# Kernel optimization log

Measured on AMD Instinct MI355X. Metric: run time of the kernel, lower is better.

Reference implementation:

```python
import jax, jax.numpy as jnp
import numpy as np

B, C, NS, NT = 8, 256, 16384, 2048
KQ = 64            # self-attention key/query dim
D = 64             # cond_conv_feat_dim
W0, W1, W2 = D * D, D * D, D * 1   # dynamic weight sizes (predict_mask=True)
B0, B1, B2 = D, D, 1
CTRL = W0 + W1 + W2 + B0 + B1 + B2  # 8385


def setup_inputs() -> dict:
    key = jax.random.key(0)
    ks = jax.random.split(key, 9)
    return {
        "scene_feat": jax.random.normal(ks[0], (B, C, NS), jnp.float32),
        "template_feat": jax.random.normal(ks[1], (B, C, NT), jnp.float32),
        # SelfAttention 1x1-conv (= linear over channels) weights
        "q_w": jax.random.normal(ks[2], (KQ, C), jnp.float32) * 0.02,
        "k_w": jax.random.normal(ks[3], (KQ, C), jnp.float32) * 0.02,
        "v_w": jax.random.normal(ks[4], (C, C), jnp.float32) * 0.02,
        # projection head of SimpleAggregator: Conv1d(3*C -> D, k=1) + ReLU
        "proj_w": jax.random.normal(ks[5], (D, 3 * C), jnp.float32) * 0.02,
        "proj_b": jnp.zeros((D,), jnp.float32),
        # controller head: Linear(C -> CTRL), init normal(std=0.01), bias 0
        "ctrl_w": jax.random.normal(ks[6], (CTRL, C), jnp.float32) * 0.01,
        "ctrl_b": jnp.zeros((CTRL,), jnp.float32),
    }


def _self_attention(x, q_w, k_w, v_w):
    # x: [B, C, N] -> [B, C_out, N]
    q = jnp.einsum("kc,bcn->bnk", q_w, x)          # [B, N, KQ]
    k = jnp.einsum("kc,bcn->bkn", k_w, x)          # [B, KQ, N]
    v = jnp.einsum("oc,bcn->bno", v_w, x)          # [B, N, C_out]
    attn = jax.nn.softmax(jnp.einsum("bnk,bkm->bnm", q / jnp.sqrt(jnp.float32(KQ)), k), axis=-1)
    y = jnp.einsum("bnm,bmo->bon", attn, v)        # [B, C_out, N]
    return y


def reference(scene_feat, template_feat, q_w, k_w, v_w, proj_w, proj_b, ctrl_w, ctrl_b):
    # ---- SimpleAggregator (self-attention on template inside) ----
    t_sa = _self_attention(template_feat, q_w, k_w, v_w)       # [B, C, NT]
    t_max = jnp.max(t_sa, axis=-1, keepdims=True)              # [B, C, 1]
    aggr = jnp.concatenate(
        [scene_feat - t_max, scene_feat * t_max, scene_feat], axis=1
    )                                                          # [B, 3C, NS]
    x = jax.nn.relu(jnp.einsum("oc,bcn->bon", proj_w, aggr) + proj_b[None, :, None])  # [B, D, NS]

    # ---- controller head on ORIGINAL template_feat max-pooled ----
    pooled = jnp.max(template_feat, axis=-1)                   # [B, C]
    params = pooled @ ctrl_w.T + ctrl_b                        # [B, CTRL]

    # parse_dynamic_params: splits = weights then biases
    o = 0
    w0 = params[:, o:o + W0].reshape(B, D, D); o += W0
    w1 = params[:, o:o + W1].reshape(B, D, D); o += W1
    w2 = params[:, o:o + W2].reshape(B, 1, D); o += W2
    b0 = params[:, o:o + B0]; o += B0
    b1 = params[:, o:o + B1]; o += B1
    b2 = params[:, o:o + B2]

    # per-sample dynamic 1x1 convs (groups=batch trick == batched GEMM)
    x = jax.nn.relu(jnp.einsum("boi,bin->bon", w0, x) + b0[:, :, None])
    x = jax.nn.relu(jnp.einsum("boi,bin->bon", w1, x) + b1[:, :, None])
    x = jnp.einsum("boi,bin->bon", w2, x) + b2[:, :, None]    # [B, 1, NS], no relu (mask layer)
    return x.reshape(B, NS)
```

## Files before the change

kernel.cpp:

```cpp
#include <hip/hip_runtime.h>
#include <hip/hip_fp8.h>


typedef __attribute__((ext_vector_type(8))) short short8;
typedef __attribute__((ext_vector_type(4))) short short4v;
typedef __attribute__((ext_vector_type(4))) float f32x4;

__device__ __forceinline__ unsigned short f2bf(float f){
  unsigned u = __float_as_uint(f);
  u += 0x7FFFu + ((u >> 16) & 1u);
  return (unsigned short)(u >> 16);
}
__device__ __forceinline__ unsigned char f2e4m3(float f){
  return __hip_fp8_e4m3(f).__x;
}
__device__ __forceinline__ unsigned fenc(float f){
  unsigned u = __float_as_uint(f);
  return (u & 0x80000000u) ? ~u : (u | 0x80000000u);
}
__device__ __forceinline__ float fdec(unsigned k){
  unsigned u = (k & 0x80000000u) ? (k & 0x7FFFFFFFu) : ~k;
  return __uint_as_float(u);
}

__global__ __launch_bounds__(256) void k0w(const float* __restrict__ qw,
    const float* __restrict__ kw, const float* __restrict__ vw,
    unsigned short* __restrict__ Wbf, unsigned* __restrict__ tmaxe,
    unsigned* __restrict__ pooledEnc){
  if (blockIdx.x == 0){
    const unsigned ninf = fenc(-3.0e38f);
    for (int i = threadIdx.x; i < 2048; i += 256){
      tmaxe[i] = 0u;
      pooledEnc[i] = ninf;
    }
  }
  const int e = (blockIdx.x * 256 + threadIdx.x) * 4;
  const int row = e >> 8, c = e & 255;
  const float* src;
  float scl = 1.0f;
  if (row < 64){ src = qw + row * 256 + c; scl = 0.125f; }
  else if (row < 128){ src = kw + (row - 64) * 256 + c; }
  else { src = vw + (row - 128) * 256 + c; }
  float4 v = *(const float4*)src;
  short4v o;
  o[0] = (short)f2bf(v.x * scl); o[1] = (short)f2bf(v.y * scl);
  o[2] = (short)f2bf(v.z * scl); o[3] = (short)f2bf(v.w * scl);
  *(short4v*)(Wbf + e) = o;
}

__global__ __launch_bounds__(256) void k0_tt(const float* __restrict__ T,
    unsigned short* __restrict__ Tt, unsigned* __restrict__ pooledEnc){
  const int b = blockIdx.x, nt = blockIdx.y, ct = blockIdx.z;
  const int n0 = nt * 128, c0 = ct * 32;
  const int tid = threadIdx.x;
  __shared__ float Ls[32][129];
  const int cr = tid >> 3, nq = tid & 7;
  const float* src = T + ((size_t)b * 256 + c0 + cr) * 2048 + n0 + nq * 16;
  float4 v0 = ((const float4*)src)[0];
  float4 v1 = ((const float4*)src)[1];
  float4 v2 = ((const float4*)src)[2];
  float4 v3 = ((const float4*)src)[3];
  float mx = fmaxf(fmaxf(fmaxf(v0.x, v0.y), fmaxf(v0.z, v0.w)),
                   fmaxf(fmaxf(v1.x, v1.y), fmaxf(v1.z, v1.w)));
  mx = fmaxf(mx, fmaxf(fmaxf(fmaxf(v2.x, v2.y), fmaxf(v2.z, v2.w)),
                       fmaxf(fmaxf(v3.x, v3.y), fmaxf(v3.z, v3.w))));
  mx = fmaxf(mx, __shfl_xor(mx, 1));
  mx = fmaxf(mx, __shfl_xor(mx, 2));
  mx = fmaxf(mx, __shfl_xor(mx, 4));
  if (nq == 0) atomicMax(&pooledEnc[b * 256 + c0 + cr], fenc(mx));
  float* lr = &Ls[cr][nq * 16];
  *(float4*)lr = v0; *(float4*)(lr + 4) = v1;
  *(float4*)(lr + 8) = v2; *(float4*)(lr + 12) = v3;
  __syncthreads();
  const int nr = tid >> 1, ch = tid & 1;
  unsigned short ob[16];
  #pragma unroll
  for (int j = 0; j < 16; j++) ob[j] = f2bf(Ls[ch * 16 + j][nr]);
  unsigned short* dst = Tt + ((size_t)b * 2048 + n0 + nr) * 256 + c0 + ch * 16;
  *(short8*)dst = *(short8*)&ob[0];
  *(short8*)(dst + 8) = *(short8*)&ob[8];
}

__global__ __launch_bounds__(256) void k23_qkv_params(
    const unsigned short* __restrict__ Wbf, const unsigned short* __restrict__ Tt,
    unsigned short* __restrict__ qo, unsigned short* __restrict__ ko,
    unsigned char* __restrict__ vt8,
    const unsigned* __restrict__ pooledEnc, const float* __restrict__ cw,
    const float* __restrict__ cb, float* __restrict__ params){
  const int wg = blockIdx.x;
  const int tid = threadIdx.x, lane = tid & 63, w = tid >> 6;
  if (wg >= 512){
    __shared__ float P[8 * 256];
    for (int i = tid; i < 2048; i += 256) P[i] = fdec(pooledEnc[i]);
    __syncthreads();
    const int r = (wg - 512) * 4 + w;
    if (r >= 8385) return;
    float4 c4 = ((const float4*)(cw + (size_t)r * 256))[lane];
    float bias = cb[r];
    #pragma unroll
    for (int b = 0; b < 8; b++){
      const float* pbp = P + b * 256 + lane * 4;
      float s = c4.x * pbp[0] + c4.y * pbp[1] + c4.z * pbp[2] + c4.w * pbp[3];
      #pragma unroll
      for (int d = 1; d < 64; d <<= 1) s += __shfl_xor(s, d);
      if (lane == 0) params[b * 8385 + r] = s + bias;
    }
    return;
  }
  const int b = wg & 7, nt = wg >> 3;
  const int n0 = nt * 32;
  const int l15 = lane & 15, g = lane >> 4;
  const unsigned short* Tb = Tt + (size_t)b * 2048 * 256;

  f32x4 aqk[2][2], av[4][2];
  #pragma unroll
  for (int i = 0; i < 2; i++)
    #pragma unroll
    for (int nf = 0; nf < 2; nf++) aqk[i][nf] = (f32x4){0.f,0.f,0.f,0.f};
  #pragma unroll
  for (int j = 0; j < 4; j++)
    #pragma unroll
    for (int nf = 0; nf < 2; nf++) av[j][nf] = (f32x4){0.f,0.f,0.f,0.f};

  #pragma unroll 2
  for (int kc = 0; kc < 8; kc++){
    short8 bfr[2];
    #pragma unroll
    for (int nf = 0; nf < 2; nf++)
      bfr[nf] = *(const short8*)(Tb + (size_t)(n0 + nf * 16 + l15) * 256 + kc * 32 + g * 8);
    short8 aq[2];
    #pragma unroll
    for (int i = 0; i < 2; i++)
      aq[i] = *(const short8*)(Wbf + (size_t)((2 * w + i) * 16 + l15) * 256 + kc * 32 + g * 8);
    short8 afv[4];
    #pragma unroll
    for (int j = 0; j < 4; j++)
      afv[j] = *(const short8*)(Wbf + (size_t)(128 + (4 * w + j) * 16 + l15) * 256 + kc * 32 + g * 8);
    #pragma unroll
    for (int i = 0; i < 2; i++)
      #pragma unroll
      for (int nf = 0; nf < 2; nf++)
        aqk[i][nf] = __builtin_amdgcn_mfma_f32_16x16x32_bf16(aq[i], bfr[nf], aqk[i][nf], 0, 0, 0);
    #pragma unroll
    for (int j = 0; j < 4; j++)
      #pragma unroll
      for (int nf = 0; nf < 2; nf++)
        av[j][nf] = __builtin_amdgcn_mfma_f32_16x16x32_bf16(bfr[nf], afv[j], av[j][nf], 0, 0, 0);
  }
  unsigned short* qk = (w < 2) ? qo : ko;
  #pragma unroll
  for (int i = 0; i < 2; i++)
    #pragma unroll
    for (int nf = 0; nf < 2; nf++){
      int n = n0 + nf * 16 + l15;
      int cbase = (w & 1) * 32 + i * 16 + g * 4;
      short4v pk;
      #pragma unroll
      for (int r = 0; r < 4; r++) pk[r] = (short)f2bf(aqk[i][nf][r]);
      *(short4v*)(qk + ((size_t)b * 2048 + n) * 64 + cbase) = pk;
    }
  #pragma unroll
  for (int j = 0; j < 4; j++)
    #pragma unroll
    for (int nf = 0; nf < 2; nf++){
      int o = (4 * w + j) * 16 + l15;
      int nb2 = n0 + nf * 16 + g * 4;
      unsigned pv8 = 0;
      #pragma unroll
      for (int r = 0; r < 4; r++)
        pv8 |= (unsigned)f2e4m3(av[j][nf][r]) << (8 * r);
      *(unsigned*)(vt8 + ((size_t)b * 256 + o) * 2048 + nb2) = pv8;
    }
}

__global__ __launch_bounds__(512, 4) void kA_scores(
    const unsigned short* __restrict__ Qg, const unsigned short* __restrict__ Kg,
    unsigned char* __restrict__ Pg, float* __restrict__ sbuf,
    int b0, int bshift){
  const int wg = blockIdx.x;
  const int bmask = (1 << bshift) - 1;
  const int b = b0 + (wg & bmask);
  const int q0 = (wg >> bshift) * 32;
  const int tid = threadIdx.x, lane = tid & 63, w = tid >> 6;
  const int l15 = lane & 15, g = lane >> 4;
  __shared__ float wsum[32][8];
  const unsigned short* Qb = Qg + (size_t)b * 2048 * 64;
  const unsigned short* Kb = Kg + (size_t)b * 2048 * 64;
  unsigned char* Pb = Pg + (size_t)(wg & bmask) * 2048 * 2048;

  short8 qf[2][2];
  #pragma unroll
  for (int qi = 0; qi < 2; qi++)
    #pragma unroll
    for (int kc = 0; kc < 2; kc++)
      qf[qi][kc] = *(const short8*)(Qb + (size_t)(q0 + qi * 16 + l15) * 64 + kc * 32 + g * 8);

  float ps[2] = {0.f, 0.f};

  const int wm0 = w * 256;
  #pragma unroll
  for (int mt = 0; mt < 4; ++mt){
    const int mb = wm0 + mt * 64;
    short8 kf[4][2];
    #pragma unroll
    for (int mi = 0; mi < 4; mi++)
      #pragma unroll
      for (int kc = 0; kc < 2; kc++)
        kf[mi][kc] = *(const short8*)(Kb + (size_t)(mb + mi * 16 + l15) * 64 + kc * 32 + g * 8);
    #pragma unroll
    for (int qi = 0; qi < 2; qi++){
      f32x4 sa[4];
      #pragma unroll
      for (int mi = 0; mi < 4; mi++) sa[mi] = (f32x4){0.f,0.f,0.f,0.f};
      #pragma unroll
      for (int mi = 0; mi < 4; mi++)
        #pragma unroll
        for (int kc = 0; kc < 2; kc++)
          sa[mi] = __builtin_amdgcn_mfma_f32_16x16x32_bf16(kf[mi][kc], qf[qi][kc], sa[mi], 0, 0, 0);
      #pragma unroll
      for (int mi = 0; mi < 4; mi++){
        unsigned pk8 = 0;
        #pragma unroll
        for (int r = 0; r < 4; r++){
          float p = __expf(sa[mi][r]);
          ps[qi] += p;
          pk8 |= (unsigned)f2e4m3(p) << (8 * r);
        }
        *(unsigned*)(Pb + (size_t)(q0 + qi * 16 + l15) * 2048 + mb + mi * 16 + g * 4) = pk8;
      }
    }
  }
  #pragma unroll
  for (int qi = 0; qi < 2; qi++){
    float t = ps[qi];
    t += __shfl_xor(t, 16);
    t += __shfl_xor(t, 32);
    if (lane < 16) wsum[qi * 16 + l15][w] = t;
  }
  __syncthreads();
  if (tid < 32){
    float t = 0.f;
    #pragma unroll
    for (int i = 0; i < 8; i++) t += wsum[tid][i];
    sbuf[(size_t)b * 2048 + q0 + tid] = t;
  }
}

__global__ __launch_bounds__(256, 4) void kB_pv(
    const unsigned char* __restrict__ Pg, const unsigned char* __restrict__ Vt,
    const float* __restrict__ sbuf, unsigned* __restrict__ tmaxe,
    int b0, int bshift){
  const int wg = blockIdx.x;
  const int bmask = (1 << bshift) - 1;
  const int b = b0 + (wg & bmask);
  const int rest = wg >> bshift;
  const int oh = rest & 1;
  const int n0 = (rest >> 1) * 64;
  const int tid = threadIdx.x, lane = tid & 63, w = tid >> 6;
  const int l15 = lane & 15, g = lane >> 4;
  __shared__ __align__(16) unsigned char smem[2][12288];

  const unsigned char* Pb = Pg + (size_t)(wg & bmask) * 2048 * 2048;
  const unsigned char* Vb = Vt + ((size_t)b * 256 + oh * 128) * 2048;

  f32x4 acc[4][2];
  #pragma unroll
  for (int ni = 0; ni < 4; ni++)
    #pragma unroll
    for (int oi = 0; oi < 2; oi++) acc[ni][oi] = (f32x4){0.f,0.f,0.f,0.f};

  const unsigned char* psrc[3];
  {
    #pragma unroll
    for (int k = 0; k < 3; k++){
      int d = k * 4096 + w * 1024 + lane * 16;
      if (k < 1){
        int row = d >> 6;
        int colB = (d & 63) ^ ((row & 3) << 4);
        psrc[k] = Pb + (size_t)(n0 + row) * 2048 + colB;
      } else {
        int dv = d - 4096;
        int row = dv >> 6;
        int colB = (dv & 63) ^ ((row & 3) << 4);
        psrc[k] = Vb + (size_t)row * 2048 + colB;
      }
    }
  }
  auto ISSUE = [&](int m0, int bufIdx){
    #pragma unroll
    for (int k = 0; k < 3; k++){
      unsigned char* dst = &smem[bufIdx][k * 4096 + w * 1024];
      __builtin_amdgcn_global_load_lds(
          (const __attribute__((address_space(1))) void*)(psrc[k] + m0),
          (__attribute__((address_space(3))) void*)dst, 16, 0, 0);
    }
  };

  ISSUE(0, 0);
  __syncthreads();

  for (int t = 0; t < 32; ++t){
    unsigned char* cur = smem[t & 1];
    if (t < 31) ISSUE((t + 1) * 64, (t + 1) & 1);
    long af[4][2], bf[2][2];
    #pragma unroll
    for (int ni = 0; ni < 4; ni++)
      #pragma unroll
      for (int kc = 0; kc < 2; kc++){
        int row = ni * 16 + l15;
        af[ni][kc] = *(const long*)(cur + row * 64 + ((kc * 32 + g * 8) ^ ((row & 3) << 4)));
      }
    #pragma unroll
    for (int oi = 0; oi < 2; oi++)
      #pragma unroll
      for (int kc = 0; kc < 2; kc++){
        int row = w * 32 + oi * 16 + l15;
        bf[oi][kc] = *(const long*)(cur + 4096 + row * 64 + ((kc * 32 + g * 8) ^ ((row & 3) << 4)));
      }
    #pragma unroll
    for (int ni = 0; ni < 4; ni++)
      #pragma unroll
      for (int oi = 0; oi < 2; oi++)
        #pragma unroll
        for (int kc = 0; kc < 2; kc++)
          acc[ni][oi] = __builtin_amdgcn_mfma_f32_16x16x32_fp8_fp8(af[ni][kc], bf[oi][kc], acc[ni][oi], 0, 0, 0);
    if (t < 31)
      __syncthreads();
  }
  float inv[4][4];
  #pragma unroll
  for (int ni = 0; ni < 4; ni++)
    #pragma unroll
    for (int r = 0; r < 4; r++)
      inv[ni][r] = 1.0f / sbuf[(size_t)b * 2048 + n0 + ni * 16 + g * 4 + r];
  #pragma unroll
  for (int oi = 0; oi < 2; oi++){
    float cm = -1e30f;
    #pragma unroll
    for (int ni = 0; ni < 4; ni++)
      #pragma unroll
      for (int r = 0; r < 4; r++)
        cm = fmaxf(cm, acc[ni][oi][r] * inv[ni][r]);
    cm = fmaxf(cm, __shfl_xor(cm, 16));
    cm = fmaxf(cm, __shfl_xor(cm, 32));
    if (lane < 16)
      atomicMax(&tmaxe[b * 256 + oh * 128 + w * 32 + oi * 16 + lane], fenc(cm));
  }
}

__global__ __launch_bounds__(256) void k5_weff(const float* __restrict__ proj_w,
    const float* __restrict__ proj_b, const unsigned* __restrict__ tmaxe,
    const float* __restrict__ params, unsigned short* __restrict__ weff,
    float* __restrict__ beff, unsigned short* __restrict__ w0b,
    unsigned short* __restrict__ w1b){
  const int b = blockIdx.y, o = blockIdx.x;
  const int c = threadIdx.x;
  float t = fdec(tmaxe[b * 256 + c]);
  float p0 = proj_w[o * 768 + c];
  float p1 = proj_w[o * 768 + 256 + c];
  float p2 = proj_w[o * 768 + 512 + c];
  weff[((size_t)b * 64 + o) * 256 + c] = f2bf(p0 + p1 * t + p2);
  float s = p0 * t;
  #pragma unroll
  for (int d = 1; d < 64; d <<= 1) s += __shfl_xor(s, d);
  __shared__ float sm[4];
  if ((c & 63) == 0) sm[c >> 6] = s;
  __syncthreads();
  if (c == 0) beff[b * 64 + o] = proj_b[o] - (sm[0] + sm[1] + sm[2] + sm[3]);
  if (c < 64)        w0b[((size_t)b * 64 + o) * 64 + c] = f2bf(params[b * 8385 + o * 64 + c]);
  else if (c < 128)  w1b[((size_t)b * 64 + o) * 64 + (c - 64)] = f2bf(params[b * 8385 + 4096 + o * 64 + (c - 64)]);
}

__global__ __launch_bounds__(512) void k6_main(const float* __restrict__ Sg,
    const unsigned short* __restrict__ weff, const float* __restrict__ beff,
    const unsigned short* __restrict__ w0b, const unsigned short* __restrict__ w1b,
    const float* __restrict__ params, float* __restrict__ out){
  const int b = blockIdx.y, nt = blockIdx.x;
  const int n0 = nt * 256;
  const int tid = threadIdx.x, lane = tid & 63, w = tid >> 6;
  const int l15 = lane & 15, g = lane >> 4;
  __shared__ __align__(16) unsigned char smem[65536];
  unsigned short* H0 = (unsigned short*)smem;
  unsigned char*  Ub = smem + 32768;
  unsigned short* H1 = (unsigned short*)Ub;

  const float* Sb = Sg + (size_t)b * 256 * 16384;
  const unsigned short* We = weff + (size_t)b * 64 * 256;
  f32x4 a0[4][2];
  #pragma unroll
  for (int mi = 0; mi < 4; mi++)
    #pragma unroll
    for (int ni = 0; ni < 2; ni++) a0[mi][ni] = (f32x4){0.f,0.f,0.f,0.f};

  const int scc = tid & 31;
  const int snb = (tid >> 5) * 16;
  const float* src0 = Sb + (size_t)scc * 16384 + n0 + snb;
  float4 v0 = ((const float4*)src0)[0];
  float4 v1 = ((const float4*)src0)[1];
  float4 v2 = ((const float4*)src0)[2];
  float4 v3 = ((const float4*)src0)[3];
  for (int k0 = 0; k0 < 256; k0 += 32){
    float vals[16] = {v0.x,v0.y,v0.z,v0.w, v1.x,v1.y,v1.z,v1.w,
                      v2.x,v2.y,v2.z,v2.w, v3.x,v3.y,v3.z,v3.w};
    #pragma unroll
    for (int j = 0; j < 16; j++){
      int n = snb + j;
      unsigned byteo = ((unsigned)(n * 64 + scc * 2)) ^ ((unsigned)((n >> 1) & 3) << 4);
      *(unsigned short*)(Ub + byteo) = f2bf(vals[j]);
    }
    if (k0 < 224){
      const float* nsrc = Sb + (size_t)(k0 + 32 + scc) * 16384 + n0 + snb;
      v0 = ((const float4*)nsrc)[0];
      v1 = ((const float4*)nsrc)[1];
      v2 = ((const float4*)nsrc)[2];
      v3 = ((const float4*)nsrc)[3];
    }
    __syncthreads();
    short8 bf0[2];
    #pragma unroll
    for (int ni = 0; ni < 2; ni++){
      int n = w * 32 + ni * 16 + l15;
      bf0[ni] = *(const short8*)(Ub + (((unsigned)(n * 64 + g * 16)) ^ ((unsigned)((n >> 1) & 3) << 4)));
    }
    #pragma unroll
    for (int mi = 0; mi < 4; mi++){
      short8 af = *(const short8*)(We + (mi * 16 + l15) * 256 + k0 + g * 8);
      #pragma unroll
      for (int ni = 0; ni < 2; ni++)
        a0[mi][ni] = __builtin_amdgcn_mfma_f32_16x16x32_bf16(af, bf0[ni], a0[mi][ni], 0, 0, 0);
    }
    __syncthreads();
  }
  const float* be = beff + b * 64;
  #pragma unroll
  for (int mi = 0; mi < 4; mi++)
    #pragma unroll
    for (int ni = 0; ni < 2; ni++){
      int n = w * 32 + ni * 16 + l15;
      unsigned base = ((unsigned)(n * 128 + mi * 32 + g * 8)) ^ ((unsigned)((n & 7) << 4));
      unsigned short hh[4];
      #pragma unroll
      for (int r = 0; r < 4; r++){
        int o = mi * 16 + g * 4 + r;
        hh[r] = f2bf(fmaxf(a0[mi][ni][r] + be[o], 0.f));
      }
      *(unsigned*)((unsigned char*)H0 + base)     = (unsigned)hh[0] | ((unsigned)hh[1] << 16);
      *(unsigned*)((unsigned char*)H0 + base + 4) = (unsigned)hh[2] | ((unsigned)hh[3] << 16);
    }
  __syncthreads();
  f32x4 a1[4][2];
  #pragma unroll
  for (int mi = 0; mi < 4; mi++)
    #pragma unroll
    for (int ni = 0; ni < 2; ni++) a1[mi][ni] = (f32x4){0.f,0.f,0.f,0.f};
  const unsigned short* W0 = w0b + (size_t)b * 4096;
  #pragma unroll
  for (int ks = 0; ks < 2; ks++){
    short8 bfh[2];
    #pragma unroll
    for (int ni = 0; ni < 2; ni++){
      int n = w * 32 + ni * 16 + l15;
      unsigned off = ((unsigned)(n * 128 + ks * 64 + g * 16)) ^ ((unsigned)((n & 7) << 4));
      bfh[ni] = *(const short8*)((unsigned char*)H0 + off);
    }
    #pragma unroll
    for (int mi = 0; mi < 4; mi++){
      short8 af = *(const short8*)(W0 + (mi * 16 + l15) * 64 + ks * 32 + g * 8);
      #pragma unroll
      for (int ni = 0; ni < 2; ni++)
        a1[mi][ni] = __builtin_amdgcn_mfma_f32_16x16x32_bf16(af, bfh[ni], a1[mi][ni], 0, 0, 0);
    }
  }
  const float* pp = params + (size_t)b * 8385;
  const float* b0p = pp + 8256;
  #pragma unroll
  for (int mi = 0; mi < 4; mi++)
    #pragma unroll
    for (int ni = 0; ni < 2; ni++){
      int n = w * 32 + ni * 16 + l15;
      unsigned base = ((unsigned)(n * 128 + mi * 32 + g * 8)) ^ ((unsigned)((n & 7) << 4));
      unsigned short hh[4];
      #pragma unroll
      for (int r = 0; r < 4; r++){
        int o = mi * 16 + g * 4 + r;
        hh[r] = f2bf(fmaxf(a1[mi][ni][r] + b0p[o], 0.f));
      }
      *(unsigned*)((unsigned char*)H1 + base)     = (unsigned)hh[0] | ((unsigned)hh[1] << 16);
      *(unsigned*)((unsigned char*)H1 + base + 4) = (unsigned)hh[2] | ((unsigned)hh[3] << 16);
    }
  __syncthreads();
  f32x4 a2[4][2];
  #pragma unroll
  for (int mi = 0; mi < 4; mi++)
    #pragma unroll
    for (int ni = 0; ni < 2; ni++) a2[mi][ni] = (f32x4){0.f,0.f,0.f,0.f};
  const unsigned short* W1 = w1b + (size_t)b * 4096;
  #pragma unroll
  for (int ks = 0; ks < 2; ks++){
    short8 bfh[2];
    #pragma unroll
    for (int ni = 0; ni < 2; ni++){
      int n = w * 32 + ni * 16 + l15;
      unsigned off = ((unsigned)(n * 128 + ks * 64 + g * 16)) ^ ((unsigned)((n & 7) << 4));
      bfh[ni] = *(const short8*)((unsigned char*)H1 + off);
    }
    #pragma unroll
    for (int mi = 0; mi < 4; mi++){
      short8 af = *(const short8*)(W1 + (mi * 16 + l15) * 64 + ks * 32 + g * 8);
      #pragma unroll
      for (int ni = 0; ni < 2; ni++)
        a2[mi][ni] = __builtin_amdgcn_mfma_f32_16x16x32_bf16(af, bfh[ni], a2[mi][ni], 0, 0, 0);
    }
  }
  const float* b1p = pp + 8320;
  const float* w2p = pp + 8192;
  float b2v = pp[8384];
  #pragma unroll
  for (int ni = 0; ni < 2; ni++){
    float t = 0.f;
    #pragma unroll
    for (int mi = 0; mi < 4; mi++)
      #pragma unroll
      for (int r = 0; r < 4; r++){
        int o = mi * 16 + g * 4 + r;
        t += w2p[o] * fmaxf(a2[mi][ni][r] + b1p[o], 0.f);
      }
    t += __shfl_xor(t, 16);
    t += __shfl_xor(t, 32);
    if (lane < 16)
      out[(size_t)b * 16384 + n0 + w * 32 + ni * 16 + l15] = t + b2v;
  }
}

extern "C" void kernel_launch(void* const* d_in, const int* in_sizes, int n_in,
                              void* d_out, int out_size, void* d_ws, size_t ws_size,
                              hipStream_t stream){
  const float* scene = (const float*)d_in[0];
  const float* tmpl  = (const float*)d_in[1];
  const float* qw    = (const float*)d_in[2];
  const float* kw    = (const float*)d_in[3];
  const float* vw    = (const float*)d_in[4];
  const float* pw    = (const float*)d_in[5];
  const float* pb    = (const float*)d_in[6];
  const float* cw    = (const float*)d_in[7];
  const float* cb    = (const float*)d_in[8];
  float* out = (float*)d_out;
  char* ws = (char*)d_ws;

  unsigned short* Q      = (unsigned short*)(ws + 0);
  unsigned short* K      = (unsigned short*)(ws + (2u << 20));
  unsigned char*  V8     = (unsigned char*)(ws + (4u << 20));
  unsigned*       pooledEnc = (unsigned*)(ws + (12u << 20));
  unsigned*       tmaxe  = (unsigned*)(ws + (12u << 20) + 8192);
  float*          params = (float*)(ws + (12u << 20) + 16384);
  unsigned short* w0b    = (unsigned short*)(ws + (13u << 20));
  unsigned short* w1b    = (unsigned short*)(ws + (13u << 20) + 65536);
  unsigned short* weff   = (unsigned short*)(ws + (13u << 20) + 131072);
  float*          beff   = (float*)(ws + (13u << 20) + 131072 + 262144);
  float*          sbuf   = (float*)(ws + (14u << 20));
  unsigned short* Wbf    = (unsigned short*)(ws + (14u << 20) + 131072);
  unsigned char*  P8buf  = (unsigned char*)(ws + (16u << 20));
  unsigned short* Tt     = (unsigned short*)P8buf;

  const size_t pPerBatch = (size_t)2048 * 2048;
  size_t avail = ws_size > (16u << 20) ? ws_size - (16u << 20) : 0;
  int nb = 8, bshift = 3;
  while (nb > 1 && (size_t)nb * pPerBatch > avail){ nb >>= 1; bshift--; }

  k0w<<<dim3(96), dim3(256), 0, stream>>>(qw, kw, vw, Wbf, tmaxe, pooledEnc);
  k0_tt<<<dim3(8, 16, 8), dim3(256), 0, stream>>>(tmpl, Tt, pooledEnc);
  k23_qkv_params<<<dim3(512 + 2097), dim3(256), 0, stream>>>(Wbf, Tt, Q, K, V8,
                                                             pooledEnc, cw, cb, params);
  for (int b0 = 0; b0 < 8; b0 += nb){
    kA_scores<<<dim3(64 * nb), dim3(512), 0, stream>>>(Q, K, P8buf, sbuf, b0, bshift);
    kB_pv<<<dim3(64 * nb), dim3(256), 0, stream>>>(P8buf, V8, sbuf, tmaxe, b0, bshift);
  }
  k5_weff<<<dim3(64, 8), dim3(256), 0, stream>>>(pw, pb, tmaxe, params, weff, beff, w0b, w1b);
  k6_main<<<dim3(64, 8), dim3(512), 0, stream>>>(scene, weff, beff, w0b, w1b, params, out);
}
```

Baseline: 140.1 us.

## Use 16x16x128 scaled FP8 MFMA in PV kernel and fold weight-cast launch

The PV kernel now uses the gfx950 scaled MFMA with K=128 and unit E8M0 scales. K tiles double to 128 bytes per row, with the LDS buffers and swizzle doubled to match, so it runs half as many loop iterations and barriers. Occupancy is lowered to 3 waves per SIMD to make room for the larger shared memory. Separately, the weight bf16-cast kernel is merged into the template transpose kernel as extra blocks, and the max-buffer init is replaced by a memset, removing one launch.

```diff
diff --git a/kernel.cpp b/kernel.cpp
--- a/kernel.cpp
+++ b/kernel.cpp
@@ -5,6 +5,7 @@
 typedef __attribute__((ext_vector_type(8))) short short8;
 typedef __attribute__((ext_vector_type(4))) short short4v;
 typedef __attribute__((ext_vector_type(4))) float f32x4;
+typedef __attribute__((ext_vector_type(8))) int int8v;
 
 __device__ __forceinline__ unsigned short f2bf(float f){
   unsigned u = __float_as_uint(f);
@@ -23,36 +24,29 @@
   return __uint_as_float(u);
 }
 
-__global__ __launch_bounds__(256) void k0w(const float* __restrict__ qw,
-    const float* __restrict__ kw, const float* __restrict__ vw,
-    unsigned short* __restrict__ Wbf, unsigned* __restrict__ tmaxe,
-    unsigned* __restrict__ pooledEnc){
-  if (blockIdx.x == 0){
-    const unsigned ninf = fenc(-3.0e38f);
-    for (int i = threadIdx.x; i < 2048; i += 256){
-      tmaxe[i] = 0u;
-      pooledEnc[i] = ninf;
-    }
-  }
-  const int e = (blockIdx.x * 256 + threadIdx.x) * 4;
-  const int row = e >> 8, c = e & 255;
-  const float* src;
-  float scl = 1.0f;
-  if (row < 64){ src = qw + row * 256 + c; scl = 0.125f; }
-  else if (row < 128){ src = kw + (row - 64) * 256 + c; }
-  else { src = vw + (row - 128) * 256 + c; }
-  float4 v = *(const float4*)src;
-  short4v o;
-  o[0] = (short)f2bf(v.x * scl); o[1] = (short)f2bf(v.y * scl);
-  o[2] = (short)f2bf(v.z * scl); o[3] = (short)f2bf(v.w * scl);
-  *(short4v*)(Wbf + e) = o;
-}
-
 __global__ __launch_bounds__(256) void k0_tt(const float* __restrict__ T,
-    unsigned short* __restrict__ Tt, unsigned* __restrict__ pooledEnc){
-  const int b = blockIdx.x, nt = blockIdx.y, ct = blockIdx.z;
+    unsigned short* __restrict__ Tt, unsigned* __restrict__ pooledEnc,
+    const float* __restrict__ qw, const float* __restrict__ kw,
+    const float* __restrict__ vw, unsigned short* __restrict__ Wbf){
+  const int wg = blockIdx.x;
+  const int tid = threadIdx.x;
+  if (wg >= 1024){
+    const int e = ((wg - 1024) * 256 + tid) * 4;
+    const int row = e >> 8, c = e & 255;
+    const float* src;
+    float scl = 1.0f;
+    if (row < 64){ src = qw + row * 256 + c; scl = 0.125f; }
+    else if (row < 128){ src = kw + (row - 64) * 256 + c; }
+    else { src = vw + (row - 128) * 256 + c; }
+    float4 v = *(const float4*)src;
+    short4v o;
+    o[0] = (short)f2bf(v.x * scl); o[1] = (short)f2bf(v.y * scl);
+    o[2] = (short)f2bf(v.z * scl); o[3] = (short)f2bf(v.w * scl);
+    *(short4v*)(Wbf + e) = o;
+    return;
+  }
+  const int b = wg & 7, nt = (wg >> 3) & 15, ct = wg >> 7;
   const int n0 = nt * 128, c0 = ct * 32;
-  const int tid = threadIdx.x;
   __shared__ float Ls[32][129];
   const int cr = tid >> 3, nq = tid & 7;
   const float* src = T + ((size_t)b * 256 + c0 + cr) * 2048 + n0 + nq * 16;
@@ -246,7 +240,7 @@
   }
 }
 
-__global__ __launch_bounds__(256, 4) void kB_pv(
+__global__ __launch_bounds__(256, 3) void kB_pv(
     const unsigned char* __restrict__ Pg, const unsigned char* __restrict__ Vt,
     const float* __restrict__ sbuf, unsigned* __restrict__ tmaxe,
     int b0, int bshift){
@@ -258,7 +252,7 @@
   const int n0 = (rest >> 1) * 64;
   const int tid = threadIdx.x, lane = tid & 63, w = tid >> 6;
   const int l15 = lane & 15, g = lane >> 4;
-  __shared__ __align__(16) unsigned char smem[2][12288];
+  __shared__ __align__(32) unsigned char smem[2][24576];
 
   const unsigned char* Pb = Pg + (size_t)(wg & bmask) * 2048 * 2048;
   const unsigned char* Vb = Vt + ((size_t)b * 256 + oh * 128) * 2048;
@@ -269,26 +263,26 @@
     #pragma unroll
     for (int oi = 0; oi < 2; oi++) acc[ni][oi] = (f32x4){0.f,0.f,0.f,0.f};
 
-  const unsigned char* psrc[3];
+  const unsigned char* psrc[6];
   {
     #pragma unroll
-    for (int k = 0; k < 3; k++){
+    for (int k = 0; k < 6; k++){
       int d = k * 4096 + w * 1024 + lane * 16;
-      if (k < 1){
-        int row = d >> 6;
-        int colB = (d & 63) ^ ((row & 3) << 4);
+      if (k < 2){
+        int row = d >> 7;
+        int colB = (d & 127) ^ ((row & 3) << 5);
         psrc[k] = Pb + (size_t)(n0 + row) * 2048 + colB;
       } else {
-        int dv = d - 4096;
-        int row = dv >> 6;
-        int colB = (dv & 63) ^ ((row & 3) << 4);
+        int dv = d - 8192;
+        int row = dv >> 7;
+        int colB = (dv & 127) ^ ((row & 3) << 5);
         psrc[k] = Vb + (size_t)row * 2048 + colB;
       }
     }
   }
   auto ISSUE = [&](int m0, int bufIdx){
     #pragma unroll
-    for (int k = 0; k < 3; k++){
+    for (int k = 0; k < 6; k++){
       unsigned char* dst = &smem[bufIdx][k * 4096 + w * 1024];
       __builtin_amdgcn_global_load_lds(
           (const __attribute__((address_space(1))) void*)(psrc[k] + m0),
@@ -299,32 +293,28 @@
   ISSUE(0, 0);
   __syncthreads();
 
-  for (int t = 0; t < 32; ++t){
+  const int SC = 0x7F7F7F7F;
+  for (int t = 0; t < 16; ++t){
     unsigned char* cur = smem[t & 1];
-    if (t < 31) ISSUE((t + 1) * 64, (t + 1) & 1);
-    long af[4][2], bf[2][2];
+    if (t < 15) ISSUE((t + 1) * 128, (t + 1) & 1);
+    int8v af[4], bf[2];
+    #pragma unroll
+    for (int ni = 0; ni < 4; ni++){
+      int row = ni * 16 + l15;
+      af[ni] = *(const int8v*)(cur + row * 128 + ((g * 32) ^ ((row & 3) << 5)));
+    }
+    #pragma unroll
+    for (int oi = 0; oi < 2; oi++){
+      int row = w * 32 + oi * 16 + l15;
+      bf[oi] = *(const int8v*)(cur + 8192 + row * 128 + ((g * 32) ^ ((row & 3) << 5)));
+    }
     #pragma unroll
     for (int ni = 0; ni < 4; ni++)
       #pragma unroll
-      for (int kc = 0; kc < 2; kc++){
-        int row = ni * 16 + l15;
-        af[ni][kc] = *(const long*)(cur + row * 64 + ((kc * 32 + g * 8) ^ ((row & 3) << 4)));
-      }
-    #pragma unroll
-    for (int oi = 0; oi < 2; oi++)
-      #pragma unroll
-      for (int kc = 0; kc < 2; kc++){
-        int row = w * 32 + oi * 16 + l15;
-        bf[oi][kc] = *(const long*)(cur + 4096 + row * 64 + ((kc * 32 + g * 8) ^ ((row & 3) << 4)));
-      }
-    #pragma unroll
-    for (int ni = 0; ni < 4; ni++)
-      #pragma unroll
       for (int oi = 0; oi < 2; oi++)
-        #pragma unroll
-        for (int kc = 0; kc < 2; kc++)
-          acc[ni][oi] = __builtin_amdgcn_mfma_f32_16x16x32_fp8_fp8(af[ni][kc], bf[oi][kc], acc[ni][oi], 0, 0, 0);
-    if (t < 31)
+        acc[ni][oi] = __builtin_amdgcn_mfma_scale_f32_16x16x128_f8f6f4(
+            af[ni], bf[oi], acc[ni][oi], 0, 0, 0, SC, 0, SC);
+    if (t < 15)
       __syncthreads();
   }
   float inv[4][4];
@@ -567,8 +557,8 @@
   int nb = 8, bshift = 3;
   while (nb > 1 && (size_t)nb * pPerBatch > avail){ nb >>= 1; bshift--; }
 
-  k0w<<<dim3(96), dim3(256), 0, stream>>>(qw, kw, vw, Wbf, tmaxe, pooledEnc);
-  k0_tt<<<dim3(8, 16, 8), dim3(256), 0, stream>>>(tmpl, Tt, pooledEnc);
+  hipMemsetAsync(ws + (12u << 20), 0, 16384, stream);
+  k0_tt<<<dim3(1120), dim3(256), 0, stream>>>(tmpl, Tt, pooledEnc, qw, kw, vw, Wbf);
   k23_qkv_params<<<dim3(512 + 2097), dim3(256), 0, stream>>>(Wbf, Tt, Q, K, V8,
                                                              pooledEnc, cw, cb, params);
   for (int b0 = 0; b0 < 8; b0 += nb){
```

Result: faster. 130.7 us (-6.7%).
